# Kernel optimization log

Hardware: AMD Instinct MI355X
Metric: run time of the kernel (lower is better)

The kernel has to match this reference:

```python
import jax, jax.numpy as jnp
import numpy as np

N_HEAD = 16
NEG_BIG = 1e10  # matches the torch module's -10000000000.0 additive mask


def setup_inputs() -> dict:
    key = jax.random.key(0)
    k1, k2, k3 = jax.random.split(key, 3)
    B, T, D = 2, 2048, 1024
    x = jax.random.normal(k1, (B, T, D), dtype=jnp.float32)
    W_attn = jax.random.normal(k2, (D, 3 * D), dtype=jnp.float32) * 0.02
    b_attn = jnp.zeros((3 * D,), dtype=jnp.float32)
    W_proj = jax.random.normal(k3, (D, D), dtype=jnp.float32) * 0.02
    b_proj = jnp.zeros((D,), dtype=jnp.float32)
    return {"x": x, "W_attn": W_attn, "b_attn": b_attn,
            "W_proj": W_proj, "b_proj": b_proj}


def reference(x, W_attn, b_attn, W_proj, b_proj):
    B, T, D = x.shape
    H = N_HEAD
    dh = D // H
    # c_attn: fused qkv projection
    qkv = x @ W_attn + b_attn                      # [B, T, 3D]
    q, k, v = jnp.split(qkv, 3, axis=-1)
    # split heads -> [B, H, T, dh]
    q = q.reshape(B, T, H, dh).transpose(0, 2, 1, 3)
    k = k.reshape(B, T, H, dh).transpose(0, 2, 1, 3)
    v = v.reshape(B, T, H, dh).transpose(0, 2, 1, 3)
    # scores [B, H, T, T]
    w = jnp.einsum("bhqd,bhkd->bhqk", q, k)
    w = w / jnp.sqrt(jnp.float32(dh))              # scale=True
    # causal additive mask: w*b - 1e10*(1-b), b = lower-triangular ones
    bias = jnp.tril(jnp.ones((T, T), dtype=w.dtype))
    w = w * bias - NEG_BIG * (1.0 - bias)
    w = jax.nn.softmax(w, axis=-1)
    a = jnp.einsum("bhqk,bhkd->bhqd", w, v)        # [B, H, T, dh]
    # merge heads
    a = a.transpose(0, 2, 1, 3).reshape(B, T, D)
    # c_proj
    return a @ W_proj + b_proj
```

## Files before the change

### kernel.cpp

```cpp
#include <hip/hip_runtime.h>
#include <hip/hip_bf16.h>


typedef unsigned short u16;
typedef unsigned int u32;
typedef __attribute__((ext_vector_type(4))) float f32x4;
typedef __attribute__((ext_vector_type(16))) float f32x16;
typedef __attribute__((ext_vector_type(8))) short bf16x8;
typedef __attribute__((ext_vector_type(4))) int i32x4;

__device__ __forceinline__ u16 f2bf(float f) {
  unsigned u = __builtin_bit_cast(unsigned, f);
  u += 0x7FFFu + ((u >> 16) & 1u);
  return (u16)(u >> 16);
}

__device__ __forceinline__ u32 pack_bf2(float lo, float hi) {
  return (u32)f2bf(lo) | ((u32)f2bf(hi) << 16);
}

__device__ __forceinline__ void gl_lds16(const u16* g, u16* l) {
  __builtin_amdgcn_global_load_lds(
      (const __attribute__((address_space(1))) void*)g,
      (__attribute__((address_space(3))) void*)l, 16, 0, 0);
}

__global__ __launch_bounds__(256) void cast_bf16_kernel(const float* __restrict__ in,
                                                        u16* __restrict__ out, int n4) {
  int i = blockIdx.x * 256 + threadIdx.x;
  if (i < n4) {
    float4 f = reinterpret_cast<const float4*>(in)[i];
    ushort4 o;
    o.x = f2bf(f.x); o.y = f2bf(f.y); o.z = f2bf(f.z); o.w = f2bf(f.w);
    reinterpret_cast<ushort4*>(out)[i] = o;
  }
}

__global__ __launch_bounds__(256) void transpose_cast(const float* __restrict__ in,
                                                      u16* __restrict__ out, int R, int C) {
  __shared__ float tile[32][33];
  const int c0 = blockIdx.x * 32, r0 = blockIdx.y * 32;
  const int tx = threadIdx.x, ty = threadIdx.y;
#pragma unroll
  for (int i = 0; i < 4; ++i)
    tile[ty + 8 * i][tx] = in[(size_t)(r0 + ty + 8 * i) * C + c0 + tx];
  __syncthreads();
#pragma unroll
  for (int i = 0; i < 4; ++i)
    out[(size_t)(c0 + ty + 8 * i) * R + r0 + tx] = f2bf(tile[tx][ty + 8 * i]);
}

__global__ __launch_bounds__(256) void gemm_qkv(
    const u16* __restrict__ A, const u16* __restrict__ Bt, const float* __restrict__ bias,
    u16* __restrict__ Qh, u16* __restrict__ Kh, u16* __restrict__ VhT, int K) {
  __shared__ u16 As[128 * 32];
  __shared__ u16 Bs[128 * 32];
  const int tid = threadIdx.x;
  const int wave = tid >> 6, lane = tid & 63;
  const int kg = lane >> 4, rr = lane & 15;
  const int wm = wave >> 1, wn = wave & 1;
  const int nwg = gridDim.x * gridDim.y;
  const int lin = blockIdx.y * gridDim.x + blockIdx.x;
  const int swz = (lin & 7) * (nwg >> 3) + (lin >> 3);
  const int bx = swz % gridDim.x, by = swz / gridDim.x;
  const int rowA0 = by * 128, colB0 = bx * 128;

  const f32x4 z4 = {0.f, 0.f, 0.f, 0.f};
  f32x4 acc[4][4];
#pragma unroll
  for (int i = 0; i < 4; ++i)
#pragma unroll
    for (int j = 0; j < 4; ++j) acc[i][j] = z4;

  const int r_st = tid >> 2;
  const int c_st = (tid & 3) * 8;

  for (int k0 = 0; k0 < K; k0 += 32) {
#pragma unroll
    for (int i = 0; i < 2; ++i) {
      gl_lds16(A + (size_t)(rowA0 + i * 64 + r_st) * K + k0 + c_st,
               As + (i * 256 + (wave << 6)) * 8);
      gl_lds16(Bt + (size_t)(colB0 + i * 64 + r_st) * K + k0 + c_st,
               Bs + (i * 256 + (wave << 6)) * 8);
    }
    __syncthreads();

    bf16x8 af[4], bfr[4];
#pragma unroll
    for (int mi = 0; mi < 4; ++mi)
      af[mi] = *reinterpret_cast<const bf16x8*>(&As[(wm * 64 + mi * 16 + rr) * 32 + kg * 8]);
#pragma unroll
    for (int ni = 0; ni < 4; ++ni)
      bfr[ni] = *reinterpret_cast<const bf16x8*>(&Bs[(wn * 64 + ni * 16 + rr) * 32 + kg * 8]);
#pragma unroll
    for (int mi = 0; mi < 4; ++mi)
#pragma unroll
      for (int ni = 0; ni < 4; ++ni)
        acc[mi][ni] = __builtin_amdgcn_mfma_f32_16x16x32_bf16(af[mi], bfr[ni], acc[mi][ni], 0, 0, 0);
    __syncthreads();
  }

#pragma unroll
  for (int mi = 0; mi < 4; ++mi) {
#pragma unroll
    for (int ni = 0; ni < 4; ++ni) {
      const int col = colB0 + wn * 64 + ni * 16 + rr;
      const float bcol = bias[col];
      f32x4 a = acc[mi][ni];
#pragma unroll
      for (int v = 0; v < 4; ++v) {
        const int row = rowA0 + wm * 64 + mi * 16 + kg * 4 + v;
        const float val = a[v] + bcol;
        const int b = row >> 11, t = row & 2047;
        const int which = col >> 10, d = col & 1023;
        const int h = d >> 6, dd = d & 63;
        const size_t bh = (size_t)(b * 16 + h);
        if (which == 0)
          Qh[(bh * 2048 + t) * 64 + dd] = f2bf(val * 0.125f);
        else if (which == 1)
          Kh[(bh * 2048 + t) * 64 + dd] = f2bf(val);
        else
          VhT[(bh * 64 + dd) * 2048 + t] = f2bf(val);
      }
    }
  }
}

__global__ __launch_bounds__(256) void gemm_proj(
    const u16* __restrict__ A, const u16* __restrict__ Bt, const float* __restrict__ bias,
    float* __restrict__ outF, int N, int K) {
  __shared__ u16 As[128 * 32];
  __shared__ u16 Bs[64 * 32];
  const int tid = threadIdx.x;
  const int wave = tid >> 6, lane = tid & 63;
  const int kg = lane >> 4, rr = lane & 15;
  const int nwg = gridDim.x * gridDim.y;
  const int lin = blockIdx.y * gridDim.x + blockIdx.x;
  const int swz = (lin & 7) * (nwg >> 3) + (lin >> 3);
  const int bx = swz % gridDim.x, by = swz / gridDim.x;
  const int rowA0 = by * 128, colB0 = bx * 64;

  const f32x4 z4 = {0.f, 0.f, 0.f, 0.f};
  f32x4 acc[2][4];
#pragma unroll
  for (int i = 0; i < 2; ++i)
#pragma unroll
    for (int j = 0; j < 4; ++j) acc[i][j] = z4;

  const int r_st = tid >> 2;
  const int c_st = (tid & 3) * 8;

  for (int k0 = 0; k0 < K; k0 += 32) {
#pragma unroll
    for (int i = 0; i < 2; ++i)
      gl_lds16(A + (size_t)(rowA0 + i * 64 + r_st) * K + k0 + c_st,
               As + (i * 256 + (wave << 6)) * 8);
    gl_lds16(Bt + (size_t)(colB0 + r_st) * K + k0 + c_st, Bs + (wave << 6) * 8);
    __syncthreads();

    bf16x8 af[2], bfr[4];
#pragma unroll
    for (int mi = 0; mi < 2; ++mi)
      af[mi] = *reinterpret_cast<const bf16x8*>(&As[(wave * 32 + mi * 16 + rr) * 32 + kg * 8]);
#pragma unroll
    for (int ni = 0; ni < 4; ++ni)
      bfr[ni] = *reinterpret_cast<const bf16x8*>(&Bs[(ni * 16 + rr) * 32 + kg * 8]);
#pragma unroll
    for (int mi = 0; mi < 2; ++mi)
#pragma unroll
      for (int ni = 0; ni < 4; ++ni)
        acc[mi][ni] = __builtin_amdgcn_mfma_f32_16x16x32_bf16(af[mi], bfr[ni], acc[mi][ni], 0, 0, 0);
    __syncthreads();
  }

#pragma unroll
  for (int mi = 0; mi < 2; ++mi) {
#pragma unroll
    for (int ni = 0; ni < 4; ++ni) {
      const int col = colB0 + ni * 16 + rr;
      const float bcol = bias[col];
      f32x4 a = acc[mi][ni];
#pragma unroll
      for (int v = 0; v < 4; ++v) {
        const int row = rowA0 + wave * 32 + mi * 16 + kg * 4 + v;
        outF[(size_t)row * N + col] = a[v] + bcol;
      }
    }
  }
}

__global__ __launch_bounds__(256) void attn_fwd(const u16* __restrict__ Qh,
                                                const u16* __restrict__ Kh,
                                                const u16* __restrict__ VhT,
                                                u16* __restrict__ Ab) {
  __shared__ float Ol[4][64][33];
  __shared__ float Ml[4][2][32];
  const int tid = threadIdx.x;
  const int wave = tid >> 6, lane = tid & 63;
  const int lq = lane & 31, hi = lane >> 5;
  const int blk = blockIdx.x;
  const int qi = blk >> 5;
  const int bh = blk & 31;
  const int qtile = 63 - qi;
  const int q0 = qtile * 32;
  const int myq = q0 + lq;
  const size_t kvbase = (size_t)bh * 2048;

  const int n64 = (q0 + 32 + 63) >> 6;
  const int base = n64 >> 2, rem = n64 & 3;
  const int cnt = base + (wave < rem ? 1 : 0);
  const int start = wave * base + (wave < rem ? wave : rem);

  bf16x8 qf[4];
  {
    const u16* qptr = Qh + (kvbase + q0 + lq) * 64 + hi * 8;
#pragma unroll
    for (int ks = 0; ks < 4; ++ks)
      qf[ks] = *reinterpret_cast<const bf16x8*>(qptr + ks * 16);
  }

  f32x16 oA, oB;
#pragma unroll
  for (int i = 0; i < 16; ++i) { oA[i] = 0.f; oB[i] = 0.f; }
  float m = -1e30f, l = 0.f;

  for (int kvb = start; kvb < start + cnt; ++kvb) {
    const int kv0 = kvb * 64;

    const u16* kptr = Kh + (kvbase + kv0 + lq) * 64 + hi * 8;
    bf16x8 kfA[4], kfB[4];
#pragma unroll
    for (int ks = 0; ks < 4; ++ks) {
      kfA[ks] = *reinterpret_cast<const bf16x8*>(kptr + ks * 16);
      kfB[ks] = *reinterpret_cast<const bf16x8*>(kptr + 2048 + ks * 16);
    }
    const u16* vptr = VhT + ((size_t)bh * 64 + lq) * 2048 + kv0 + hi * 8;
    bf16x8 vfA[4], vfB[4];
#pragma unroll
    for (int ks = 0; ks < 4; ++ks) {
      vfA[ks] = *reinterpret_cast<const bf16x8*>(vptr + ks * 16);
      vfB[ks] = *reinterpret_cast<const bf16x8*>(vptr + 32 * 2048 + ks * 16);
    }

    f32x16 sA, sB;
#pragma unroll
    for (int i = 0; i < 16; ++i) { sA[i] = 0.f; sB[i] = 0.f; }
#pragma unroll
    for (int ks = 0; ks < 4; ++ks)
      sA = __builtin_amdgcn_mfma_f32_32x32x16_bf16(kfA[ks], qf[ks], sA, 0, 0, 0);
#pragma unroll
    for (int ks = 0; ks < 4; ++ks)
      sB = __builtin_amdgcn_mfma_f32_32x32x16_bf16(kfB[ks], qf[ks], sB, 0, 0, 0);

    if (kvb == n64 - 1) {
#pragma unroll
      for (int r = 0; r < 16; ++r) {
        const int kvA = kv0 + (r & 3) + 8 * (r >> 2) + 4 * hi;
        if (kvA > myq) sA[r] = -1e30f;
        if (kvA + 32 > myq) sB[r] = -1e30f;
      }
    }

    float pmax = -1e30f;
#pragma unroll
    for (int r = 0; r < 16; ++r) pmax = fmaxf(pmax, fmaxf(sA[r], sB[r]));
    pmax = fmaxf(pmax, __shfl_xor(pmax, 32));
    if (!__all(pmax - m <= 8.0f)) {
      const float mn = fmaxf(m, pmax);
      const float sc = __expf(m - mn);
      l *= sc;
      oA *= sc;
      oB *= sc;
      m = mn;
    }
    float rsum = 0.f;
#pragma unroll
    for (int r = 0; r < 16; ++r) {
      const float pa = __expf(sA[r] - m);
      const float pb = __expf(sB[r] - m);
      sA[r] = pa; sB[r] = pb;
      rsum += pa + pb;
    }
    rsum += __shfl_xor(rsum, 32);
    l += rsum;

    u32 pkA[8], pkB[8];
#pragma unroll
    for (int i = 0; i < 8; ++i) {
      pkA[i] = pack_bf2(sA[2 * i], sA[2 * i + 1]);
      pkB[i] = pack_bf2(sB[2 * i], sB[2 * i + 1]);
    }
    bf16x8 pf[4];
    {
      auto w0 = __builtin_amdgcn_permlane32_swap(pkA[0], pkA[2], false, false);
      auto w1 = __builtin_amdgcn_permlane32_swap(pkA[1], pkA[3], false, false);
      i32x4 t0 = {(int)w0[0], (int)w1[0], (int)w0[1], (int)w1[1]};
      pf[0] = __builtin_bit_cast(bf16x8, t0);
      auto w2 = __builtin_amdgcn_permlane32_swap(pkA[4], pkA[6], false, false);
      auto w3 = __builtin_amdgcn_permlane32_swap(pkA[5], pkA[7], false, false);
      i32x4 t1 = {(int)w2[0], (int)w3[0], (int)w2[1], (int)w3[1]};
      pf[1] = __builtin_bit_cast(bf16x8, t1);
      auto w4 = __builtin_amdgcn_permlane32_swap(pkB[0], pkB[2], false, false);
      auto w5 = __builtin_amdgcn_permlane32_swap(pkB[1], pkB[3], false, false);
      i32x4 t2 = {(int)w4[0], (int)w5[0], (int)w4[1], (int)w5[1]};
      pf[2] = __builtin_bit_cast(bf16x8, t2);
      auto w6 = __builtin_amdgcn_permlane32_swap(pkB[4], pkB[6], false, false);
      auto w7 = __builtin_amdgcn_permlane32_swap(pkB[5], pkB[7], false, false);
      i32x4 t3 = {(int)w6[0], (int)w7[0], (int)w6[1], (int)w7[1]};
      pf[3] = __builtin_bit_cast(bf16x8, t3);
    }

#pragma unroll
    for (int ks = 0; ks < 4; ++ks)
      oA = __builtin_amdgcn_mfma_f32_32x32x16_bf16(vfA[ks], pf[ks], oA, 0, 0, 0);
#pragma unroll
    for (int ks = 0; ks < 4; ++ks)
      oB = __builtin_amdgcn_mfma_f32_32x32x16_bf16(vfB[ks], pf[ks], oB, 0, 0, 0);
  }

  if (hi == 0) {
    Ml[wave][0][lq] = m;
    Ml[wave][1][lq] = l;
  }
#pragma unroll
  for (int r = 0; r < 16; ++r) {
    const int dhA = (r & 3) + 8 * (r >> 2) + 4 * hi;
    Ol[wave][dhA][lq] = oA[r];
    Ol[wave][dhA + 32][lq] = oB[r];
  }
  __syncthreads();

  const int col = tid >> 3;
  const int dh0 = (tid & 7) * 8;
  float mw[4];
  float M = -1e30f;
#pragma unroll
  for (int w = 0; w < 4; ++w) { mw[w] = Ml[w][0][col]; M = fmaxf(M, mw[w]); }
  float scw[4];
  float lsum = 0.f;
#pragma unroll
  for (int w = 0; w < 4; ++w) {
    scw[w] = __expf(mw[w] - M);
    lsum += scw[w] * Ml[w][1][col];
  }
  const float inv = 1.0f / lsum;
  const int b = bh >> 4, h = bh & 15;
  u16* dst = Ab + ((size_t)b * 2048 + q0 + col) * 1024 + h * 64 + dh0;
  ushort4 w0, w1;
  u16 tmp[8];
#pragma unroll
  for (int i = 0; i < 8; ++i) {
    const int dh = dh0 + i;
    float v = 0.f;
#pragma unroll
    for (int w = 0; w < 4; ++w) v += scw[w] * Ol[w][dh][col];
    tmp[i] = f2bf(v * inv);
  }
  w0.x = tmp[0]; w0.y = tmp[1]; w0.z = tmp[2]; w0.w = tmp[3];
  w1.x = tmp[4]; w1.y = tmp[5]; w1.z = tmp[6]; w1.w = tmp[7];
  *reinterpret_cast<ushort4*>(dst) = w0;
  *reinterpret_cast<ushort4*>(dst + 4) = w1;
}

extern "C" void kernel_launch(void* const* d_in, const int* in_sizes, int n_in,
                              void* d_out, int out_size, void* d_ws, size_t ws_size,
                              hipStream_t stream) {
  const float* x      = (const float*)d_in[0];
  const float* W_attn = (const float*)d_in[1];
  const float* b_attn = (const float*)d_in[2];
  const float* W_proj = (const float*)d_in[3];
  const float* b_proj = (const float*)d_in[4];
  float* out = (float*)d_out;

  u16* xb  = (u16*)d_ws;
  u16* Wat = xb + (size_t)4096 * 1024;
  u16* Wpt = Wat + (size_t)3072 * 1024;
  u16* Qh  = Wpt + (size_t)1024 * 1024;
  u16* Kh  = Qh + (size_t)4194304;
  u16* VhT = Kh + (size_t)4194304;
  u16* Ab  = VhT + (size_t)4194304;

  cast_bf16_kernel<<<4096, 256, 0, stream>>>(x, xb, 4096 * 1024 / 4);
  transpose_cast<<<dim3(96, 32), dim3(32, 8), 0, stream>>>(W_attn, Wat, 1024, 3072);
  transpose_cast<<<dim3(32, 32), dim3(32, 8), 0, stream>>>(W_proj, Wpt, 1024, 1024);
  gemm_qkv<<<dim3(24, 32), 256, 0, stream>>>(xb, Wat, b_attn, Qh, Kh, VhT, 1024);
  attn_fwd<<<dim3(2048), 256, 0, stream>>>(Qh, Kh, VhT, Ab);
  gemm_proj<<<dim3(16, 32), 256, 0, stream>>>(Ab, Wpt, b_proj, out, 1024, 1024);
}
```

Before: 225.5 us.

## Use exp2 softmax, separate V transpose, bf16 merge buffer, unified GEMM template

Several changes land together. Q is prescaled by log2(e) so the softmax uses the exp2 intrinsic instead of expf, and bf16 packing uses the hardware v_cvt_pk_bf16_f32 instruction. V is written head-major from the QKV GEMM and then transposed by a new kernel, replacing the scattered transposed stores in the GEMM epilogue. The attention kernel gains s_setprio around its MFMA blocks, loads V after the softmax, and keeps the cross-wave merge buffer in bf16 to cut LDS use. The projection GEMM now reuses the 128x128 QKV tile template. Each piece targets a different cost, and the extra launch plus bf16 partial sums add overhead and some rounding error.

```diff
diff --git a/kernel.cpp b/kernel.cpp
--- a/kernel.cpp
+++ b/kernel.cpp
@@ -15,8 +15,10 @@
   return (u16)(u >> 16);
 }
 
-__device__ __forceinline__ u32 pack_bf2(float lo, float hi) {
-  return (u32)f2bf(lo) | ((u32)f2bf(hi) << 16);
+__device__ __forceinline__ u32 cvtpk(float lo, float hi) {
+  u32 r;
+  asm("v_cvt_pk_bf16_f32 %0, %1, %2" : "=v"(r) : "v"(lo), "v"(hi));
+  return r;
 }
 
 __device__ __forceinline__ void gl_lds16(const u16* g, u16* l) {
@@ -50,9 +52,11 @@
     out[(size_t)(c0 + ty + 8 * i) * R + r0 + tx] = f2bf(tile[tx][ty + 8 * i]);
 }
 
-__global__ __launch_bounds__(256) void gemm_qkv(
+template <int MODE>
+__global__ __launch_bounds__(256) void gemm_bf16(
     const u16* __restrict__ A, const u16* __restrict__ Bt, const float* __restrict__ bias,
-    u16* __restrict__ Qh, u16* __restrict__ Kh, u16* __restrict__ VhT, int K) {
+    float* __restrict__ outF, u16* __restrict__ Qh, u16* __restrict__ Kh, u16* __restrict__ Vh,
+    int N, int K) {
   __shared__ u16 As[128 * 32];
   __shared__ u16 Bs[128 * 32];
   const int tid = threadIdx.x;
@@ -100,6 +104,7 @@
     __syncthreads();
   }
 
+  const float QS = 0.125f * 1.44269504088896f;
 #pragma unroll
   for (int mi = 0; mi < 4; ++mi) {
 #pragma unroll
@@ -111,81 +116,50 @@
       for (int v = 0; v < 4; ++v) {
         const int row = rowA0 + wm * 64 + mi * 16 + kg * 4 + v;
         const float val = a[v] + bcol;
-        const int b = row >> 11, t = row & 2047;
-        const int which = col >> 10, d = col & 1023;
-        const int h = d >> 6, dd = d & 63;
-        const size_t bh = (size_t)(b * 16 + h);
-        if (which == 0)
-          Qh[(bh * 2048 + t) * 64 + dd] = f2bf(val * 0.125f);
-        else if (which == 1)
-          Kh[(bh * 2048 + t) * 64 + dd] = f2bf(val);
-        else
-          VhT[(bh * 64 + dd) * 2048 + t] = f2bf(val);
+        if (MODE == 1) {
+          outF[(size_t)row * N + col] = val;
+        } else {
+          const int b = row >> 11, t = row & 2047;
+          const int which = col >> 10, d = col & 1023;
+          const int h = d >> 6, dd = d & 63;
+          const size_t idx = (((size_t)(b * 16 + h)) * 2048 + t) * 64 + dd;
+          if (which == 0)
+            Qh[idx] = f2bf(val * QS);
+          else if (which == 1)
+            Kh[idx] = f2bf(val);
+          else
+            Vh[idx] = f2bf(val);
+        }
       }
     }
   }
 }
 
-__global__ __launch_bounds__(256) void gemm_proj(
-    const u16* __restrict__ A, const u16* __restrict__ Bt, const float* __restrict__ bias,
-    float* __restrict__ outF, int N, int K) {
-  __shared__ u16 As[128 * 32];
-  __shared__ u16 Bs[64 * 32];
+__global__ __launch_bounds__(256) void transpose_v(const u16* __restrict__ Vh,
+                                                   u16* __restrict__ VhT) {
+  __shared__ u16 tile[64][72];
   const int tid = threadIdx.x;
-  const int wave = tid >> 6, lane = tid & 63;
-  const int kg = lane >> 4, rr = lane & 15;
-  const int nwg = gridDim.x * gridDim.y;
-  const int lin = blockIdx.y * gridDim.x + blockIdx.x;
-  const int swz = (lin & 7) * (nwg >> 3) + (lin >> 3);
-  const int bx = swz % gridDim.x, by = swz / gridDim.x;
-  const int rowA0 = by * 128, colB0 = bx * 64;
-
-  const f32x4 z4 = {0.f, 0.f, 0.f, 0.f};
-  f32x4 acc[2][4];
-#pragma unroll
-  for (int i = 0; i < 2; ++i)
-#pragma unroll
-    for (int j = 0; j < 4; ++j) acc[i][j] = z4;
-
-  const int r_st = tid >> 2;
-  const int c_st = (tid & 3) * 8;
-
-  for (int k0 = 0; k0 < K; k0 += 32) {
-#pragma unroll
-    for (int i = 0; i < 2; ++i)
-      gl_lds16(A + (size_t)(rowA0 + i * 64 + r_st) * K + k0 + c_st,
-               As + (i * 256 + (wave << 6)) * 8);
-    gl_lds16(Bt + (size_t)(colB0 + r_st) * K + k0 + c_st, Bs + (wave << 6) * 8);
-    __syncthreads();
-
-    bf16x8 af[2], bfr[4];
-#pragma unroll
-    for (int mi = 0; mi < 2; ++mi)
-      af[mi] = *reinterpret_cast<const bf16x8*>(&As[(wave * 32 + mi * 16 + rr) * 32 + kg * 8]);
-#pragma unroll
-    for (int ni = 0; ni < 4; ++ni)
-      bfr[ni] = *reinterpret_cast<const bf16x8*>(&Bs[(ni * 16 + rr) * 32 + kg * 8]);
-#pragma unroll
-    for (int mi = 0; mi < 2; ++mi)
-#pragma unroll
-      for (int ni = 0; ni < 4; ++ni)
-        acc[mi][ni] = __builtin_amdgcn_mfma_f32_16x16x32_bf16(af[mi], bfr[ni], acc[mi][ni], 0, 0, 0);
-    __syncthreads();
-  }
-
-#pragma unroll
-  for (int mi = 0; mi < 2; ++mi) {
-#pragma unroll
-    for (int ni = 0; ni < 4; ++ni) {
-      const int col = colB0 + ni * 16 + rr;
-      const float bcol = bias[col];
-      f32x4 a = acc[mi][ni];
-#pragma unroll
-      for (int v = 0; v < 4; ++v) {
-        const int row = rowA0 + wave * 32 + mi * 16 + kg * 4 + v;
-        outF[(size_t)row * N + col] = a[v] + bcol;
-      }
-    }
+  const int t0 = blockIdx.x * 64;
+  const int bh = blockIdx.y;
+  const u16* src = Vh + ((size_t)bh * 2048 + t0) * 64;
+  {
+    const int ty = tid >> 2, tx = (tid & 3) * 16;
+    *reinterpret_cast<bf16x8*>(&tile[ty][tx]) =
+        *reinterpret_cast<const bf16x8*>(src + ty * 64 + tx);
+    *reinterpret_cast<bf16x8*>(&tile[ty][tx + 8]) =
+        *reinterpret_cast<const bf16x8*>(src + ty * 64 + tx + 8);
+  }
+  __syncthreads();
+  {
+    const int dd = tid >> 2, toff = (tid & 3) * 16;
+    bf16x8 v0, v1;
+#pragma unroll
+    for (int j = 0; j < 8; ++j) v0[j] = (short)tile[toff + j][dd];
+#pragma unroll
+    for (int j = 0; j < 8; ++j) v1[j] = (short)tile[toff + 8 + j][dd];
+    u16* dst = VhT + ((size_t)bh * 64 + dd) * 2048 + t0 + toff;
+    *reinterpret_cast<bf16x8*>(dst) = v0;
+    *reinterpret_cast<bf16x8*>(dst + 8) = v1;
   }
 }
 
@@ -193,7 +167,7 @@
                                                 const u16* __restrict__ Kh,
                                                 const u16* __restrict__ VhT,
                                                 u16* __restrict__ Ab) {
-  __shared__ float Ol[4][64][33];
+  __shared__ u16 Olq[4][32][72];
   __shared__ float Ml[4][2][32];
   const int tid = threadIdx.x;
   const int wave = tid >> 6, lane = tid & 63;
@@ -234,23 +208,18 @@
       kfA[ks] = *reinterpret_cast<const bf16x8*>(kptr + ks * 16);
       kfB[ks] = *reinterpret_cast<const bf16x8*>(kptr + 2048 + ks * 16);
     }
-    const u16* vptr = VhT + ((size_t)bh * 64 + lq) * 2048 + kv0 + hi * 8;
-    bf16x8 vfA[4], vfB[4];
-#pragma unroll
-    for (int ks = 0; ks < 4; ++ks) {
-      vfA[ks] = *reinterpret_cast<const bf16x8*>(vptr + ks * 16);
-      vfB[ks] = *reinterpret_cast<const bf16x8*>(vptr + 32 * 2048 + ks * 16);
-    }
 
     f32x16 sA, sB;
 #pragma unroll
     for (int i = 0; i < 16; ++i) { sA[i] = 0.f; sB[i] = 0.f; }
+    __builtin_amdgcn_s_setprio(1);
 #pragma unroll
     for (int ks = 0; ks < 4; ++ks)
       sA = __builtin_amdgcn_mfma_f32_32x32x16_bf16(kfA[ks], qf[ks], sA, 0, 0, 0);
 #pragma unroll
     for (int ks = 0; ks < 4; ++ks)
       sB = __builtin_amdgcn_mfma_f32_32x32x16_bf16(kfB[ks], qf[ks], sB, 0, 0, 0);
+    __builtin_amdgcn_s_setprio(0);
 
     if (kvb == n64 - 1) {
 #pragma unroll
@@ -267,7 +236,7 @@
     pmax = fmaxf(pmax, __shfl_xor(pmax, 32));
     if (!__all(pmax - m <= 8.0f)) {
       const float mn = fmaxf(m, pmax);
-      const float sc = __expf(m - mn);
+      const float sc = __builtin_amdgcn_exp2f(m - mn);
       l *= sc;
       oA *= sc;
       oB *= sc;
@@ -276,19 +245,27 @@
     float rsum = 0.f;
 #pragma unroll
     for (int r = 0; r < 16; ++r) {
-      const float pa = __expf(sA[r] - m);
-      const float pb = __expf(sB[r] - m);
+      const float pa = __builtin_amdgcn_exp2f(sA[r] - m);
+      const float pb = __builtin_amdgcn_exp2f(sB[r] - m);
       sA[r] = pa; sB[r] = pb;
       rsum += pa + pb;
     }
     rsum += __shfl_xor(rsum, 32);
     l += rsum;
 
+    const u16* vptr = VhT + ((size_t)bh * 64 + lq) * 2048 + kv0 + hi * 8;
+    bf16x8 vfA[4], vfB[4];
+#pragma unroll
+    for (int ks = 0; ks < 4; ++ks) {
+      vfA[ks] = *reinterpret_cast<const bf16x8*>(vptr + ks * 16);
+      vfB[ks] = *reinterpret_cast<const bf16x8*>(vptr + 32 * 2048 + ks * 16);
+    }
+
     u32 pkA[8], pkB[8];
 #pragma unroll
     for (int i = 0; i < 8; ++i) {
-      pkA[i] = pack_bf2(sA[2 * i], sA[2 * i + 1]);
-      pkB[i] = pack_bf2(sB[2 * i], sB[2 * i + 1]);
+      pkA[i] = cvtpk(sA[2 * i], sA[2 * i + 1]);
+      pkB[i] = cvtpk(sB[2 * i], sB[2 * i + 1]);
     }
     bf16x8 pf[4];
     {
@@ -310,56 +287,64 @@
       pf[3] = __builtin_bit_cast(bf16x8, t3);
     }
 
+    __builtin_amdgcn_s_setprio(1);
 #pragma unroll
     for (int ks = 0; ks < 4; ++ks)
       oA = __builtin_amdgcn_mfma_f32_32x32x16_bf16(vfA[ks], pf[ks], oA, 0, 0, 0);
 #pragma unroll
     for (int ks = 0; ks < 4; ++ks)
       oB = __builtin_amdgcn_mfma_f32_32x32x16_bf16(vfB[ks], pf[ks], oB, 0, 0, 0);
+    __builtin_amdgcn_s_setprio(0);
   }
 
   if (hi == 0) {
     Ml[wave][0][lq] = m;
     Ml[wave][1][lq] = l;
   }
-#pragma unroll
-  for (int r = 0; r < 16; ++r) {
-    const int dhA = (r & 3) + 8 * (r >> 2) + 4 * hi;
-    Ol[wave][dhA][lq] = oA[r];
-    Ol[wave][dhA + 32][lq] = oB[r];
+  {
+    u32* orow = reinterpret_cast<u32*>(&Olq[wave][lq][0]);
+#pragma unroll
+    for (int qd = 0; qd < 4; ++qd) {
+      const int dh0 = 8 * qd + 4 * hi;
+      orow[(dh0 >> 1) + 0] = cvtpk(oA[4 * qd + 0], oA[4 * qd + 1]);
+      orow[(dh0 >> 1) + 1] = cvtpk(oA[4 * qd + 2], oA[4 * qd + 3]);
+      orow[((dh0 + 32) >> 1) + 0] = cvtpk(oB[4 * qd + 0], oB[4 * qd + 1]);
+      orow[((dh0 + 32) >> 1) + 1] = cvtpk(oB[4 * qd + 2], oB[4 * qd + 3]);
+    }
   }
   __syncthreads();
 
   const int col = tid >> 3;
   const int dh0 = (tid & 7) * 8;
+  float M = -1e30f;
   float mw[4];
-  float M = -1e30f;
 #pragma unroll
   for (int w = 0; w < 4; ++w) { mw[w] = Ml[w][0][col]; M = fmaxf(M, mw[w]); }
+  float lsum = 0.f;
   float scw[4];
-  float lsum = 0.f;
 #pragma unroll
   for (int w = 0; w < 4; ++w) {
-    scw[w] = __expf(mw[w] - M);
+    scw[w] = __builtin_amdgcn_exp2f(mw[w] - M);
     lsum += scw[w] * Ml[w][1][col];
   }
   const float inv = 1.0f / lsum;
+  float acc8[8];
+#pragma unroll
+  for (int i = 0; i < 8; ++i) acc8[i] = 0.f;
+#pragma unroll
+  for (int w = 0; w < 4; ++w) {
+    bf16x8 ov = *reinterpret_cast<const bf16x8*>(&Olq[w][col][dh0]);
+#pragma unroll
+    for (int i = 0; i < 8; ++i) {
+      const float f = __builtin_bit_cast(float, ((u32)(u16)ov[i]) << 16);
+      acc8[i] += scw[w] * f;
+    }
+  }
   const int b = bh >> 4, h = bh & 15;
-  u16* dst = Ab + ((size_t)b * 2048 + q0 + col) * 1024 + h * 64 + dh0;
-  ushort4 w0, w1;
-  u16 tmp[8];
-#pragma unroll
-  for (int i = 0; i < 8; ++i) {
-    const int dh = dh0 + i;
-    float v = 0.f;
-#pragma unroll
-    for (int w = 0; w < 4; ++w) v += scw[w] * Ol[w][dh][col];
-    tmp[i] = f2bf(v * inv);
-  }
-  w0.x = tmp[0]; w0.y = tmp[1]; w0.z = tmp[2]; w0.w = tmp[3];
-  w1.x = tmp[4]; w1.y = tmp[5]; w1.z = tmp[6]; w1.w = tmp[7];
-  *reinterpret_cast<ushort4*>(dst) = w0;
-  *reinterpret_cast<ushort4*>(dst + 4) = w1;
+  bf16x8 outv;
+#pragma unroll
+  for (int i = 0; i < 8; ++i) outv[i] = (short)f2bf(acc8[i] * inv);
+  *reinterpret_cast<bf16x8*>(Ab + ((size_t)b * 2048 + q0 + col) * 1024 + h * 64 + dh0) = outv;
 }
 
 extern "C" void kernel_launch(void* const* d_in, const int* in_sizes, int n_in,
@@ -379,11 +364,15 @@
   u16* Kh  = Qh + (size_t)4194304;
   u16* VhT = Kh + (size_t)4194304;
   u16* Ab  = VhT + (size_t)4194304;
+  u16* Vh  = Ab;
 
   cast_bf16_kernel<<<4096, 256, 0, stream>>>(x, xb, 4096 * 1024 / 4);
   transpose_cast<<<dim3(96, 32), dim3(32, 8), 0, stream>>>(W_attn, Wat, 1024, 3072);
   transpose_cast<<<dim3(32, 32), dim3(32, 8), 0, stream>>>(W_proj, Wpt, 1024, 1024);
-  gemm_qkv<<<dim3(24, 32), 256, 0, stream>>>(xb, Wat, b_attn, Qh, Kh, VhT, 1024);
+  gemm_bf16<0><<<dim3(24, 32), 256, 0, stream>>>(xb, Wat, b_attn, nullptr, Qh, Kh, Vh,
+                                                 3072, 1024);
+  transpose_v<<<dim3(32, 32), 256, 0, stream>>>(Vh, VhT);
   attn_fwd<<<dim3(2048), 256, 0, stream>>>(Qh, Kh, VhT, Ab);
-  gemm_proj<<<dim3(16, 32), 256, 0, stream>>>(Ab, Wpt, b_proj, out, 1024, 1024);
-}
+  gemm_bf16<1><<<dim3(8, 32), 256, 0, stream>>>(Ab, Wpt, b_proj, out, nullptr, nullptr, nullptr,
+                                                1024, 1024);
+}
```

Result: no change. 227.3 us (+0.8%).
